# Performance work log

Measured on AMD Instinct MI355X. Metric: run time of the kernel, lower is better.

Reference implementation:

```python
import jax, jax.numpy as jnp
import numpy as np

N_CLASS, N_MU, OUT_DIM, K = 200, 1024, 512, 512


def setup_inputs() -> dict:
    key = jax.random.key(0)
    k1, k2, k3, k4 = jax.random.split(key, 4)
    return {
        "cls_mu_queue": jax.random.normal(k1, (N_CLASS, N_MU, OUT_DIM), jnp.float32),
        "cls_sc_queue": jax.random.uniform(k2, (N_CLASS, N_MU), jnp.float32),
        "inp_mu": jax.random.normal(k3, (K, OUT_DIM), jnp.float32),
        "inp_sc": jax.random.uniform(k4, (K, N_CLASS), jnp.float32),
        "cls_idx": jnp.arange(N_CLASS, dtype=jnp.int32),
    }


def reference(cls_mu_queue, cls_sc_queue, inp_mu, inp_sc, cls_idx):
    # Per-class sort-merge queue update (Memory._update_queue), vectorized over
    # the listed classes with vmap instead of a Python loop.
    n_mu = cls_sc_queue.shape[1]

    def merge_one(q_mu, q_sc, in_sc):
        # q_mu: [n_mu, D], q_sc: [n_mu], in_sc: [K]
        concat_sc = jnp.concatenate([q_sc, in_sc], axis=0)        # [n_mu+K]
        top_sc, top_idx = jax.lax.top_k(concat_sc, n_mu)          # sort desc, keep top n_mu
        concat_mu = jnp.concatenate([q_mu, inp_mu], axis=0)       # [n_mu+K, D]
        return concat_mu[top_idx], top_sc                         # index_select

    new_mu, new_sc = jax.vmap(merge_one)(
        cls_mu_queue[cls_idx], cls_sc_queue[cls_idx], inp_sc.T[cls_idx])

    mu_q = cls_mu_queue.at[cls_idx].set(new_mu)                   # scatter back
    sc_q = cls_sc_queue.at[cls_idx].set(new_sc)
    # Pack both updated buffers into one array: [n_class, n_mu, D+1]
    return jnp.concatenate([mu_q, sc_q[:, :, None]], axis=2)
```

## Files before the change

### kernel.cpp

```cpp
#include <hip/hip_runtime.h>
#include <hip/hip_bf16.h>

constexpr int N_CLASS = 200;
constexpr int N_MU    = 1024;
constexpr int DIM     = 512;
constexpr int KIN     = 512;
constexpr int NCAND   = N_MU + KIN;
constexpr int SORTN   = 2048;
constexpr int RPB     = 16;
constexpr int TPB     = 512;

typedef float f4 __attribute__((ext_vector_type(4)));

__global__ __launch_bounds__(1024) void sort_kernel(
    const float* __restrict__ q_sc,
    const float* __restrict__ inp_sc,
    const int*   __restrict__ cls_idx,
    int*         __restrict__ ws_idx,
    float*       __restrict__ ws_sc,
    int*         __restrict__ flags)
{
    __shared__ unsigned long long keys[SORTN];
    const int e = blockIdx.x;
    const int c = cls_idx[e];
    const int t = threadIdx.x;

    for (int i = t; i < SORTN; i += 1024) {
        unsigned long long key;
        if (i < NCAND) {
            float f = (i < N_MU) ? q_sc[(size_t)c * N_MU + i]
                                 : inp_sc[(size_t)(i - N_MU) * N_CLASS + c];
            unsigned u = __float_as_uint(f);
            unsigned s = (u & 0x80000000u) ? ~u : (u | 0x80000000u);
            unsigned inv = ~s;
            key = ((unsigned long long)inv << 32) | (unsigned)i;
        } else {
            key = 0xFFFFFFFFFFFFFFFFull;
        }
        keys[i] = key;
    }
    __syncthreads();

    for (int k = 2; k <= SORTN; k <<= 1) {
        for (int j = k >> 1; j > 0; j >>= 1) {
            const int i = ((t & ~(j - 1)) << 1) | (t & (j - 1));
            const int p = i | j;
            const bool asc = ((i & k) == 0);
            unsigned long long a = keys[i], b = keys[p];
            const bool sw = asc ? (a > b) : (a < b);
            if (sw) { keys[i] = b; keys[p] = a; }
            __syncthreads();
        }
    }

    {
        unsigned long long key = keys[t];
        const int idx = (int)(key & 0xFFFFFFFFu);
        unsigned s = ~((unsigned)(key >> 32));
        unsigned u = (s & 0x80000000u) ? (s & 0x7FFFFFFFu) : ~s;
        ws_idx[((size_t)c << 10) + t] = idx;
        ws_sc [((size_t)c << 10) + t] = __uint_as_float(u);
    }
    if (t == 0) flags[c] = 1;
}

__global__ __launch_bounds__(TPB) void out_kernel(
    const float* __restrict__ q_mu,
    const float* __restrict__ q_sc,
    const float* __restrict__ inp_mu,
    const int*   __restrict__ ws_idx,
    const float* __restrict__ ws_sc,
    const int*   __restrict__ flags,
    float*       __restrict__ out)
{
    __shared__ __align__(16) float buf[RPB * (DIM + 1)];
    __shared__ const f4* selp[RPB];
    __shared__ int       snt[RPB];
    __shared__ float     ssc[RPB];

    const int b  = blockIdx.x;
    const int c  = b >> 6;
    const int g  = b & 63;
    const int j0 = g * RPB;
    const int t  = threadIdx.x;
    const size_t rowbase = ((size_t)c << 10) + j0;

    if (t < RPB) {
        if (flags[c] != 0) {
            const int idx = ws_idx[rowbase + t];
            if (idx < N_MU) {
                selp[t] = (const f4*)(q_mu + (((size_t)c << 10) + idx) * DIM);
                snt[t] = 1;
            } else {
                selp[t] = (const f4*)(inp_mu + (size_t)(idx - N_MU) * DIM);
                snt[t] = 0;
            }
            ssc[t] = ws_sc[rowbase + t];
        } else {
            selp[t] = (const f4*)(q_mu + (rowbase + t) * DIM);
            snt[t] = 1;
            ssc[t] = q_sc[rowbase + t];
        }
    }
    __syncthreads();

#pragma unroll
    for (int j = 0; j < 4; ++j) {
        const int fq = t + TPB * j;
        const int r  = fq >> 7;
        const int q  = fq & 127;
        const f4* src = selp[r] + q;
        f4 v;
        if (snt[r]) v = __builtin_nontemporal_load(src);
        else        v = *src;
        float* d = buf + r * (DIM + 1) + q * 4;
        d[0] = v.x; d[1] = v.y; d[2] = v.z; d[3] = v.w;
    }
    if (t < RPB) buf[t * (DIM + 1) + DIM] = ssc[t];
    __syncthreads();

    f4* dst = (f4*)(out + rowbase * (DIM + 1));
#pragma unroll
    for (int j = 0; j < 5; ++j) {
        const int l = t + TPB * j;
        if (l < RPB * (DIM + 1) / 4) {
            __builtin_nontemporal_store(*(const f4*)(buf + l * 4), dst + l);
        }
    }
}

extern "C" void kernel_launch(void* const* d_in, const int* in_sizes, int n_in,
                              void* d_out, int out_size, void* d_ws, size_t ws_size,
                              hipStream_t stream) {
    const float* q_mu    = (const float*)d_in[0];
    const float* q_sc    = (const float*)d_in[1];
    const float* inp_mu  = (const float*)d_in[2];
    const float* inp_sc  = (const float*)d_in[3];
    const int*   cls_idx = (const int*)d_in[4];
    float* out = (float*)d_out;
    const int n_idx = in_sizes[4];

    constexpr size_t NQ = (size_t)N_CLASS * N_MU;
    int*   ws_idx = (int*)d_ws;
    float* ws_sc  = (float*)((char*)d_ws + NQ * 4);
    int*   flags  = (int*)((char*)d_ws + NQ * 8);

    (void)hipMemsetAsync(flags, 0, N_CLASS * sizeof(int), stream);
    sort_kernel<<<n_idx, 1024, 0, stream>>>(
        q_sc, inp_sc, cls_idx, ws_idx, ws_sc, flags);
    out_kernel<<<N_CLASS * (N_MU / RPB), TPB, 0, stream>>>(
        q_mu, q_sc, inp_mu, ws_idx, ws_sc, flags, out);
}
```

Before: 148.3 us.

## Use register-shuffle bitonic stages and overlap gather loads with stores

The sort kernel now keeps two keys per thread in registers. It runs all compare-exchange steps with stride 64 or less through wavefront shuffles, and only goes through shared memory with barriers for the larger strides. This removes most __syncthreads and LDS traffic from the bitonic sort. The output kernel splits each 16-row tile into two halves, issuing the gather loads for the second half before storing the first half. This overlaps global reads with nontemporal writes, and row pointers are resolved per thread instead of through shared metadata. The costs are more index arithmetic, extra reloads of ws_idx per element, and tighter hand-coded store offsets.

```diff
diff --git a/kernel.cpp b/kernel.cpp
--- a/kernel.cpp
+++ b/kernel.cpp
@@ -11,6 +11,7 @@
 constexpr int TPB     = 512;
 
 typedef float f4 __attribute__((ext_vector_type(4)));
+typedef unsigned long long u64;
 
 __global__ __launch_bounds__(1024) void sort_kernel(
     const float* __restrict__ q_sc,
@@ -20,46 +21,67 @@
     float*       __restrict__ ws_sc,
     int*         __restrict__ flags)
 {
-    __shared__ unsigned long long keys[SORTN];
-    const int e = blockIdx.x;
-    const int c = cls_idx[e];
+    __shared__ u64 keys[SORTN];
+    const int c = cls_idx[blockIdx.x];
     const int t = threadIdx.x;
+    const int lane = t & 63;
+    const int w    = t >> 6;
+    const int i0   = (w << 7) | (lane << 1);
+    const int i1   = i0 | 1;
 
-    for (int i = t; i < SORTN; i += 1024) {
-        unsigned long long key;
-        if (i < NCAND) {
-            float f = (i < N_MU) ? q_sc[(size_t)c * N_MU + i]
-                                 : inp_sc[(size_t)(i - N_MU) * N_CLASS + c];
-            unsigned u = __float_as_uint(f);
-            unsigned s = (u & 0x80000000u) ? ~u : (u | 0x80000000u);
-            unsigned inv = ~s;
-            key = ((unsigned long long)inv << 32) | (unsigned)i;
-        } else {
-            key = 0xFFFFFFFFFFFFFFFFull;
-        }
-        keys[i] = key;
-    }
-    __syncthreads();
+    auto make_key = [&](int i) -> u64 {
+        if (i >= NCAND) return 0xFFFFFFFFFFFFFFFFull;
+        float f = (i < N_MU) ? q_sc[(size_t)c * N_MU + i]
+                             : inp_sc[(size_t)(i - N_MU) * N_CLASS + c];
+        unsigned u = __float_as_uint(f);
+        unsigned s = (u & 0x80000000u) ? ~u : (u | 0x80000000u);
+        return ((u64)(~s) << 32) | (unsigned)i;
+    };
+    u64 e0 = make_key(i0);
+    u64 e1 = make_key(i1);
 
     for (int k = 2; k <= SORTN; k <<= 1) {
-        for (int j = k >> 1; j > 0; j >>= 1) {
-            const int i = ((t & ~(j - 1)) << 1) | (t & (j - 1));
-            const int p = i | j;
-            const bool asc = ((i & k) == 0);
-            unsigned long long a = keys[i], b = keys[p];
-            const bool sw = asc ? (a > b) : (a < b);
-            if (sw) { keys[i] = b; keys[p] = a; }
+        if (k >= 256) {
+            keys[i0] = e0; keys[i1] = e1;
             __syncthreads();
+            for (int j = k >> 1; j >= 128; j >>= 1) {
+                const int i = ((t & ~(j - 1)) << 1) | (t & (j - 1));
+                const int p = i | j;
+                const bool asc = ((i & k) == 0);
+                u64 a = keys[i], b = keys[p];
+                const bool sw = asc ? (a > b) : (a < b);
+                if (sw) { keys[i] = b; keys[p] = a; }
+                __syncthreads();
+            }
+            e0 = keys[i0]; e1 = keys[i1];
+        }
+        const bool asc = ((i0 & k) == 0);
+        for (int j = (k >> 1) < 64 ? (k >> 1) : 64; j >= 2; j >>= 1) {
+            const u64 o0 = __shfl_xor(e0, j >> 1);
+            const u64 o1 = __shfl_xor(e1, j >> 1);
+            const bool low = ((i0 & j) == 0);
+            const bool takeMin = (low == asc);
+            e0 = takeMin ? (e0 < o0 ? e0 : o0) : (e0 > o0 ? e0 : o0);
+            e1 = takeMin ? (e1 < o1 ? e1 : o1) : (e1 > o1 ? e1 : o1);
+        }
+        {
+            const u64 lo = e0 < e1 ? e0 : e1;
+            const u64 hi = e0 < e1 ? e1 : e0;
+            e0 = asc ? lo : hi;
+            e1 = asc ? hi : lo;
         }
     }
 
-    {
-        unsigned long long key = keys[t];
-        const int idx = (int)(key & 0xFFFFFFFFu);
-        unsigned s = ~((unsigned)(key >> 32));
-        unsigned u = (s & 0x80000000u) ? (s & 0x7FFFFFFFu) : ~s;
-        ws_idx[((size_t)c << 10) + t] = idx;
-        ws_sc [((size_t)c << 10) + t] = __uint_as_float(u);
+    if (w < 8) {
+        auto emit = [&](u64 key, int slot) {
+            const int idx = (int)(key & 0xFFFFFFFFu);
+            unsigned s = ~((unsigned)(key >> 32));
+            unsigned u = (s & 0x80000000u) ? (s & 0x7FFFFFFFu) : ~s;
+            ws_idx[((size_t)c << 10) + slot] = idx;
+            ws_sc [((size_t)c << 10) + slot] = __uint_as_float(u);
+        };
+        emit(e0, i0);
+        emit(e1, i1);
     }
     if (t == 0) flags[c] = 1;
 }
@@ -74,59 +96,79 @@
     float*       __restrict__ out)
 {
     __shared__ __align__(16) float buf[RPB * (DIM + 1)];
-    __shared__ const f4* selp[RPB];
-    __shared__ int       snt[RPB];
-    __shared__ float     ssc[RPB];
-
     const int b  = blockIdx.x;
     const int c  = b >> 6;
     const int g  = b & 63;
     const int j0 = g * RPB;
     const int t  = threadIdx.x;
     const size_t rowbase = ((size_t)c << 10) + j0;
+    const bool upd = (flags[c] != 0);
 
-    if (t < RPB) {
-        if (flags[c] != 0) {
-            const int idx = ws_idx[rowbase + t];
+    auto load_f4 = [&](int r, int q) -> f4 {
+        if (upd) {
+            const int idx = ws_idx[rowbase + r];
             if (idx < N_MU) {
-                selp[t] = (const f4*)(q_mu + (((size_t)c << 10) + idx) * DIM);
-                snt[t] = 1;
-            } else {
-                selp[t] = (const f4*)(inp_mu + (size_t)(idx - N_MU) * DIM);
-                snt[t] = 0;
+                return __builtin_nontemporal_load(
+                    (const f4*)(q_mu + (((size_t)c << 10) + idx) * DIM) + q);
             }
-            ssc[t] = ws_sc[rowbase + t];
-        } else {
-            selp[t] = (const f4*)(q_mu + (rowbase + t) * DIM);
-            snt[t] = 1;
-            ssc[t] = q_sc[rowbase + t];
+            return *((const f4*)(inp_mu + (size_t)(idx - N_MU) * DIM) + q);
         }
+        return __builtin_nontemporal_load(
+            (const f4*)(q_mu + (rowbase + r) * DIM) + q);
+    };
+    auto load_sc = [&](int r) -> float {
+        return upd ? ws_sc[rowbase + r] : q_sc[rowbase + r];
+    };
+    f4* dst = (f4*)(out + rowbase * (size_t)(DIM + 1));
+
+    {
+        f4 v[2];
+#pragma unroll
+        for (int j = 0; j < 2; ++j) {
+            const int fq = t + TPB * j;
+            v[j] = load_f4(fq >> 7, fq & 127);
+        }
+        float s = (t < 8) ? load_sc(t) : 0.0f;
+#pragma unroll
+        for (int j = 0; j < 2; ++j) {
+            const int fq = t + TPB * j;
+            const int r = fq >> 7, q = fq & 127;
+            float* d = buf + r * (DIM + 1) + q * 4;
+            d[0] = v[j].x; d[1] = v[j].y; d[2] = v[j].z; d[3] = v[j].w;
+        }
+        if (t < 8) buf[t * (DIM + 1) + DIM] = s;
     }
     __syncthreads();
 
+    {
+        f4 v[2];
 #pragma unroll
-    for (int j = 0; j < 4; ++j) {
-        const int fq = t + TPB * j;
-        const int r  = fq >> 7;
-        const int q  = fq & 127;
-        const f4* src = selp[r] + q;
-        f4 v;
-        if (snt[r]) v = __builtin_nontemporal_load(src);
-        else        v = *src;
-        float* d = buf + r * (DIM + 1) + q * 4;
-        d[0] = v.x; d[1] = v.y; d[2] = v.z; d[3] = v.w;
+        for (int j = 0; j < 2; ++j) {
+            const int fq = 1024 + t + TPB * j;
+            v[j] = load_f4(fq >> 7, fq & 127);
+        }
+        float s = (t < 8) ? load_sc(8 + t) : 0.0f;
+
+        __builtin_nontemporal_store(*(const f4*)(buf + t * 4),            dst + t);
+        __builtin_nontemporal_store(*(const f4*)(buf + (TPB + t) * 4),    dst + TPB + t);
+        if (t < 2)
+            __builtin_nontemporal_store(*(const f4*)(buf + (1024 + t) * 4), dst + 1024 + t);
+
+#pragma unroll
+        for (int j = 0; j < 2; ++j) {
+            const int fq = 1024 + t + TPB * j;
+            const int r = fq >> 7, q = fq & 127;
+            float* d = buf + r * (DIM + 1) + q * 4;
+            d[0] = v[j].x; d[1] = v[j].y; d[2] = v[j].z; d[3] = v[j].w;
+        }
+        if (t < 8) buf[(8 + t) * (DIM + 1) + DIM] = s;
     }
-    if (t < RPB) buf[t * (DIM + 1) + DIM] = ssc[t];
     __syncthreads();
 
-    f4* dst = (f4*)(out + rowbase * (DIM + 1));
-#pragma unroll
-    for (int j = 0; j < 5; ++j) {
-        const int l = t + TPB * j;
-        if (l < RPB * (DIM + 1) / 4) {
-            __builtin_nontemporal_store(*(const f4*)(buf + l * 4), dst + l);
-        }
-    }
+    __builtin_nontemporal_store(*(const f4*)(buf + (1026 + t) * 4),       dst + 1026 + t);
+    __builtin_nontemporal_store(*(const f4*)(buf + (1538 + t) * 4),       dst + 1538 + t);
+    if (t < 2)
+        __builtin_nontemporal_store(*(const f4*)(buf + (2050 + t) * 4),   dst + 2050 + t);
 }
 
 extern "C" void kernel_launch(void* const* d_in, const int* in_sizes, int n_in,
```

After: 143.1 us. -3.5%, faster.
